# Performance work log

Measured on AMD Instinct MI355X. Metric: run time of the kernel, lower is better.

Reference implementation:

```python
import jax, jax.numpy as jnp
import numpy as np

B, N, D, L = 64, 512, 256, 4


def setup_inputs() -> dict:
    key = jax.random.key(0)
    ks = jax.random.split(key, 10)
    scale = 1.0 / np.sqrt(D)
    x = jax.random.normal(ks[0], (B, N, D), dtype=jnp.float32)
    adj = (jax.random.uniform(ks[1], (B, N, N)) < 0.1).astype(jnp.float32)
    return {
        "x": x,
        "adj": adj,
        "w_attn_w": jax.random.normal(ks[2], (L, D, D), dtype=jnp.float32) * scale,
        "w_attn_b": jnp.zeros((L, D), dtype=jnp.float32),
        "lin0_w": jax.random.normal(ks[3], (L, D, D), dtype=jnp.float32) * scale,
        "lin0_b": jnp.zeros((L, D), dtype=jnp.float32),
        "lin1_w": jax.random.normal(ks[4], (L, D, D), dtype=jnp.float32) * scale,
        "lin1_b": jnp.zeros((L, D), dtype=jnp.float32),
        "final_w": jax.random.normal(ks[5], (D, D), dtype=jnp.float32) * scale,
        "final_b": jnp.zeros((D,), dtype=jnp.float32),
    }


def reference(x, adj, w_attn_w, w_attn_b, lin0_w, lin0_b, lin1_w, lin1_b, final_w, final_b):
    # set self-loops on the adjacency diagonal (in-place in the torch code)
    idx = jnp.arange(N)
    adj = adj.at[:, idx, idx].set(1.0)
    eye = 1e-5 * jnp.eye(N, dtype=x.dtype)
    attls = []
    for l in range(L):
        x0 = x
        # q = w_attn[l](x): torch Linear is x @ W.T + b, W: [out,in]
        q = jnp.einsum('bnd,od->bno', x, w_attn_w[l]) + w_attn_b[l]
        adj_attn = jax.nn.sigmoid(jnp.einsum('bij,bkj->bik', q, x))  # [B,N,N]
        adj_attn = (adj_attn + eye) * adj
        adj_attn = adj_attn / jnp.sum(adj_attn, axis=-1, keepdims=True)
        attls.append(adj_attn)
        x = jnp.einsum('bij,bjd->bid', adj_attn, x)
        x = jax.nn.relu(jnp.einsum('bnd,od->bno', x, lin0_w[l]) + lin0_b[l])
        x = jax.nn.relu(jnp.einsum('bnd,od->bno', x, lin1_w[l]) + lin1_b[l])
        x = x + x0
    x = jnp.einsum('bnd,od->bno', x, final_w) + final_b
    return (x, jnp.stack(attls))
```

## Files before the change

kernel.cpp:

```cpp
#include <hip/hip_runtime.h>
#include <cstdint>

#define B_ 64
#define N_ 512
#define D_ 256
#define L_ 4

typedef __bf16 bf16;
typedef __attribute__((ext_vector_type(8))) __bf16 bf16x8;
typedef __attribute__((ext_vector_type(4))) __bf16 bf16x4;
typedef __attribute__((ext_vector_type(4))) float f32x4;

#define MFMA16(a, b, c) __builtin_amdgcn_mfma_f32_16x16x32_bf16((a), (b), (c), 0, 0, 0)

__device__ __forceinline__ float sigmoidf_(float z) {
  return 1.0f / (1.0f + __expf(-z));
}


#define UIDX(u) (((size_t)(u)) * 64 + lane)

__global__ __launch_bounds__(256) void pack_w(
    const float* __restrict__ src, bf16* __restrict__ dst)
{
  const int tid = threadIdx.x, lane = tid & 63;
  const int U = blockIdx.x * 4 + (tid >> 6);
  const int m = U >> 7, u = U & 127;
  const int r16 = u >> 3, kc = u & 7;
  const int row = r16 * 16 + (lane & 15);
  const int k0 = kc * 32 + (lane >> 4) * 8;
  const float* s = src + (size_t)m * D_ * D_ + (size_t)row * D_ + k0;
  const float4 v0 = *(const float4*)s;
  const float4 v1 = *(const float4*)(s + 4);
  bf16x8 o;
  o[0] = (bf16)v0.x; o[1] = (bf16)v0.y; o[2] = (bf16)v0.z; o[3] = (bf16)v0.w;
  o[4] = (bf16)v1.x; o[5] = (bf16)v1.y; o[6] = (bf16)v1.z; o[7] = (bf16)v1.w;
  ((bf16x8*)dst)[(size_t)U * 64 + lane] = o;
}

__global__ __launch_bounds__(256) void init_pack(
    const float* __restrict__ x, bf16* __restrict__ xbpk, bf16* __restrict__ xTpk)
{
  const int tid = threadIdx.x, lane = tid & 63;
  const int U = blockIdx.x * 4 + (tid >> 6);
  const int b = U >> 9, u = U & 511;
  if (u < 256) {
    const int n = (u >> 3) * 16 + (lane & 15);
    const int d = (u & 7) * 32 + (lane >> 4) * 8;
    const float* s = x + ((size_t)(b * N_ + n)) * D_ + d;
    const float4 v0 = *(const float4*)s;
    const float4 v1 = *(const float4*)(s + 4);
    bf16x8 o;
    o[0] = (bf16)v0.x; o[1] = (bf16)v0.y; o[2] = (bf16)v0.z; o[3] = (bf16)v0.w;
    o[4] = (bf16)v1.x; o[5] = (bf16)v1.y; o[6] = (bf16)v1.z; o[7] = (bf16)v1.w;
    ((bf16x8*)xbpk)[((size_t)b * 256 + u) * 64 + lane] = o;
  } else {
    const int u2 = u - 256;
    const int d = (u2 >> 4) * 16 + (lane & 15);
    const int n = (u2 & 15) * 32 + (lane >> 4) * 8;
    bf16x8 o;
#pragma unroll
    for (int e = 0; e < 8; ++e)
      o[e] = (bf16)x[((size_t)(b * N_ + n + e)) * D_ + d];
    ((bf16x8*)xTpk)[((size_t)b * 256 + u2) * 64 + lane] = o;
  }
}

__global__ __launch_bounds__(512, 1) void gat_layer(
    const bf16* __restrict__ xbpk_in, const bf16* __restrict__ xTpk_in,
    bf16* __restrict__ xbpk_out, bf16* __restrict__ xTpk_out,
    const bf16* __restrict__ Wap, const float* __restrict__ ba,
    const bf16* __restrict__ W0p, const float* __restrict__ b0,
    const bf16* __restrict__ W1p, const float* __restrict__ b1,
    const float* __restrict__ adj, const unsigned short* __restrict__ bits_in,
    unsigned short* __restrict__ bits_out, float* __restrict__ outA)
{
  __shared__ bf16 qs[64 * 264];
  __shared__ bf16 xps[64 * 520];
  __shared__ float psum[8][64];
  __shared__ float rinvs[64];
  __shared__ unsigned int bits_s[1024];

  const int tid = threadIdx.x, w = tid >> 6, lane = tid & 63;
  const int l16 = lane & 15, quad = lane >> 4;
  const int wg = blockIdx.x;
  const int lid = (wg & 7) * 64 + (wg >> 3);
  const int b = lid >> 3;
  const int row0 = (lid & 7) * 64;

  const bf16x8* Xbp = (const bf16x8*)xbpk_in + (size_t)b * 16384;
  const bf16x8* Xtp = (const bf16x8*)xTpk_in + (size_t)b * 16384;
  bf16x8* XbpO = (bf16x8*)xbpk_out + (size_t)b * 16384;
  bf16x8* XtpO = (bf16x8*)xTpk_out + (size_t)b * 16384;
  const bf16x8* Wa8 = (const bf16x8*)Wap;
  const bf16x8* W08 = (const bf16x8*)W0p;
  const bf16x8* W18 = (const bf16x8*)W1p;

  if (bits_in) {
#pragma unroll
    for (int e = 0; e < 2; ++e) {
      const int t = tid + e * 512;
      bits_s[t] = ((const unsigned int*)bits_in)[((size_t)b * N_ + row0) * 16 + t];
    }
  }

  {
    f32x4 acc0[4][2] = {};
#pragma unroll
    for (int ks = 0; ks < 8; ++ks) {
      bf16x8 af[4];
#pragma unroll
      for (int m = 0; m < 4; ++m)
        af[m] = Xbp[UIDX(((row0 >> 4) + m) * 8 + ks)];
      bf16x8 bw[2];
#pragma unroll
      for (int i = 0; i < 2; ++i)
        bw[i] = Wa8[UIDX((2 * w + i) * 8 + ks)];
#pragma unroll
      for (int m = 0; m < 4; ++m)
#pragma unroll
        for (int i = 0; i < 2; ++i) acc0[m][i] = MFMA16(af[m], bw[i], acc0[m][i]);
    }
#pragma unroll
    for (int m = 0; m < 4; ++m)
#pragma unroll
      for (int i = 0; i < 2; ++i) {
        const int col = 32 * w + 16 * i + l16;
        const float bv = ba[col];
#pragma unroll
        for (int r = 0; r < 4; ++r)
          qs[(16 * m + quad * 4 + r) * 264 + col] = (bf16)(acc0[m][i][r] + bv);
      }
  }
  __syncthreads();

  float p[4][4] = {};
  {
    f32x4 acc1[4][4] = {};
#pragma unroll
    for (int ks = 0; ks < 8; ++ks) {
      bf16x8 af[4];
#pragma unroll
      for (int m = 0; m < 4; ++m)
        af[m] = *(const bf16x8*)&qs[(16 * m + l16) * 264 + ks * 32 + quad * 8];
      bf16x8 bx[4];
#pragma unroll
      for (int jt = 0; jt < 4; ++jt)
        bx[jt] = Xbp[UIDX((4 * w + jt) * 8 + ks)];
#pragma unroll
      for (int m = 0; m < 4; ++m)
#pragma unroll
        for (int jt = 0; jt < 4; ++jt)
          acc1[m][jt] = MFMA16(af[m], bx[jt], acc1[m][jt]);
    }
#pragma unroll
    for (int jt = 0; jt < 4; ++jt) {
      const int lcol = 64 * w + jt * 16 + l16;
      const int piece = 4 * w + jt;
#pragma unroll
      for (int m = 0; m < 4; ++m)
#pragma unroll
        for (int r = 0; r < 4; ++r) {
          const int row = 16 * m + quad * 4 + r;
          const int grow = row0 + row;
          float av;
          if (bits_in) {
            const unsigned short m16 = ((const unsigned short*)bits_s)[row * 32 + piece];
            av = (float)((m16 >> l16) & 1);
          } else {
            av = __builtin_nontemporal_load(
                adj + ((size_t)b * N_ + grow) * N_ + lcol);
          }
          const bool diag = (grow == lcol);
          if (bits_out) {
            const unsigned long long bal = __ballot(diag || av != 0.0f);
            if (l16 == 0)
              bits_out[((size_t)b * N_ + row0 + 16 * m + 4 * quad + r) * 32 + piece] =
                  (unsigned short)((bal >> (quad * 16)) & 0xFFFFull);
          }
          const float sg = sigmoidf_(acc1[m][jt][r]);
          const float v = diag ? (sg + 1e-5f) : sg * av;
          const bf16 bv = (bf16)v;
          xps[row * 520 + lcol] = bv;
          p[m][r] += (float)bv;
        }
    }
  }
#pragma unroll
  for (int m = 0; m < 4; ++m)
#pragma unroll
    for (int r = 0; r < 4; ++r) {
#pragma unroll
      for (int msk = 1; msk < 16; msk <<= 1) p[m][r] += __shfl_xor(p[m][r], msk, 64);
    }
  if (l16 == 0) {
#pragma unroll
    for (int m = 0; m < 4; ++m)
#pragma unroll
      for (int r = 0; r < 4; ++r) psum[w][16 * m + quad * 4 + r] = p[m][r];
  }
  __syncthreads();
  if (tid < 64) {
    float s = 0.0f;
#pragma unroll
    for (int ww = 0; ww < 8; ++ww) s += psum[ww][tid];
    rinvs[tid] = 1.0f / s;
  }
  __syncthreads();

  const size_t abase = ((size_t)b * N_ + row0) * N_;
#pragma unroll
  for (int e = 0; e < 16; ++e) {
    const int idx = tid + e * 512;
    const int row = idx >> 7, c4 = (idx & 127) * 4;
    const float ri = rinvs[row];
    bf16x4 pv = *(const bf16x4*)&xps[row * 520 + c4];
    f32x4 nv;
    nv[0] = (float)pv[0] * ri; nv[1] = (float)pv[1] * ri;
    nv[2] = (float)pv[2] * ri; nv[3] = (float)pv[3] * ri;
    __builtin_nontemporal_store(nv, (f32x4*)(outA + abase + (size_t)row * N_ + c4));
    bf16x4 o;
    o[0] = (bf16)nv[0]; o[1] = (bf16)nv[1]; o[2] = (bf16)nv[2]; o[3] = (bf16)nv[3];
    *(bf16x4*)&xps[row * 520 + c4] = o;
  }
  __syncthreads();

  {
    f32x4 acc3[4][2] = {};
#pragma unroll
    for (int ks = 0; ks < 16; ++ks) {
      bf16x8 af[4];
#pragma unroll
      for (int m = 0; m < 4; ++m)
        af[m] = *(const bf16x8*)&xps[(16 * m + l16) * 520 + ks * 32 + quad * 8];
      bf16x8 bt[2];
#pragma unroll
      for (int i = 0; i < 2; ++i)
        bt[i] = Xtp[UIDX((2 * w + i) * 16 + ks)];
#pragma unroll
      for (int m = 0; m < 4; ++m)
#pragma unroll
        for (int i = 0; i < 2; ++i) acc3[m][i] = MFMA16(af[m], bt[i], acc3[m][i]);
    }
#pragma unroll
    for (int m = 0; m < 4; ++m)
#pragma unroll
      for (int i = 0; i < 2; ++i) {
        const int d = 32 * w + 16 * i + l16;
#pragma unroll
        for (int r = 0; r < 4; ++r)
          qs[(16 * m + quad * 4 + r) * 264 + d] = (bf16)acc3[m][i][r];
      }
  }
  __syncthreads();

  {
    f32x4 acc[4][2] = {};
#pragma unroll
    for (int ks = 0; ks < 8; ++ks) {
      bf16x8 af[4];
#pragma unroll
      for (int m = 0; m < 4; ++m)
        af[m] = *(const bf16x8*)&qs[(16 * m + l16) * 264 + ks * 32 + quad * 8];
      bf16x8 bw[2];
#pragma unroll
      for (int i = 0; i < 2; ++i)
        bw[i] = W08[UIDX((2 * w + i) * 8 + ks)];
#pragma unroll
      for (int m = 0; m < 4; ++m)
#pragma unroll
        for (int i = 0; i < 2; ++i) acc[m][i] = MFMA16(af[m], bw[i], acc[m][i]);
    }
#pragma unroll
    for (int m = 0; m < 4; ++m)
#pragma unroll
      for (int i = 0; i < 2; ++i) {
        const int col = 32 * w + 16 * i + l16;
        const float bv = b0[col];
#pragma unroll
        for (int r = 0; r < 4; ++r)
          xps[(16 * m + quad * 4 + r) * 264 + col] = (bf16)fmaxf(acc[m][i][r] + bv, 0.0f);
      }
  }
  __syncthreads();

  {
#pragma unroll
    for (int j = 0; j < 4; ++j) {
      const int uu = w * 4 + j;
      const int rr = uu >> 3, kc = uu & 7;
      const bf16x8 v = Xbp[UIDX(((row0 >> 4) + rr) * 8 + kc)];
      *(bf16x8*)&qs[(rr * 16 + l16) * 264 + kc * 32 + quad * 8] = v;
    }
    f32x4 acc[4][2] = {};
#pragma unroll
    for (int ks = 0; ks < 8; ++ks) {
      bf16x8 af[4];
#pragma unroll
      for (int m = 0; m < 4; ++m)
        af[m] = *(const bf16x8*)&xps[(16 * m + l16) * 264 + ks * 32 + quad * 8];
      bf16x8 bw[2];
#pragma unroll
      for (int i = 0; i < 2; ++i)
        bw[i] = W18[UIDX((2 * w + i) * 8 + ks)];
#pragma unroll
      for (int m = 0; m < 4; ++m)
#pragma unroll
        for (int i = 0; i < 2; ++i) acc[m][i] = MFMA16(af[m], bw[i], acc[m][i]);
    }
    __syncthreads();

#pragma unroll
    for (int m = 0; m < 4; ++m)
#pragma unroll
      for (int i = 0; i < 2; ++i) {
        const int d = 32 * w + 16 * i + l16;
        const float bv = b1[d];
#pragma unroll
        for (int r = 0; r < 4; ++r) {
          const int nl = 16 * m + quad * 4 + r;
          const float x0 = (float)qs[nl * 264 + d];
          const float t2 = fmaxf(acc[m][i][r] + bv, 0.0f) + x0;
          qs[nl * 264 + d] = (bf16)t2;
        }
      }
    __syncthreads();

#pragma unroll
    for (int j = 0; j < 4; ++j) {
      const int uu = w * 4 + j;
      const int rr = uu >> 3, kc = uu & 7;
      const bf16x8 v = *(const bf16x8*)&qs[(rr * 16 + l16) * 264 + kc * 32 + quad * 8];
      XbpO[UIDX(((row0 >> 4) + rr) * 8 + kc)] = v;
    }
#pragma unroll
    for (int j = 0; j < 4; ++j) {
      const int uu = w * 4 + j;
      const int d16 = uu >> 1, nk = uu & 1;
      const int d = d16 * 16 + l16;
      bf16x8 v;
#pragma unroll
      for (int e = 0; e < 8; ++e)
        v[e] = qs[(nk * 32 + quad * 8 + e) * 264 + d];
      XtpO[UIDX(d16 * 16 + (row0 >> 5) + nk)] = v;
    }
  }
}

__global__ __launch_bounds__(256, 4) void final_proj(
    const bf16* __restrict__ xbpk, const bf16* __restrict__ Wfp,
    const float* __restrict__ bfv, float* __restrict__ outX)
{
  const int tid = threadIdx.x, w = tid >> 6, lane = tid & 63;
  const int l16 = lane & 15, quad = lane >> 4;
  const int wg = blockIdx.x;
  const int lid = (wg & 7) * 128 + (wg >> 3);
  const int row0g = lid * 32;
  const int b = row0g >> 9, n0 = row0g & 511;
  const bf16x8* Xbp = (const bf16x8*)xbpk + (size_t)b * 16384;
  const bf16x8* Wf8 = (const bf16x8*)Wfp;
  f32x4 acc[2][4] = {};
#pragma unroll
  for (int ks = 0; ks < 8; ++ks) {
    bf16x8 af[2];
#pragma unroll
    for (int m = 0; m < 2; ++m)
      af[m] = Xbp[UIDX(((n0 >> 4) + m) * 8 + ks)];
    bf16x8 bw[4];
#pragma unroll
    for (int i = 0; i < 4; ++i)
      bw[i] = Wf8[UIDX((4 * w + i) * 8 + ks)];
#pragma unroll
    for (int m = 0; m < 2; ++m)
#pragma unroll
      for (int i = 0; i < 4; ++i) acc[m][i] = MFMA16(af[m], bw[i], acc[m][i]);
  }
#pragma unroll
  for (int m = 0; m < 2; ++m)
#pragma unroll
    for (int i = 0; i < 4; ++i) {
      const int col = 64 * w + 16 * i + l16;
      const float bv = bfv[col];
#pragma unroll
      for (int r = 0; r < 4; ++r) {
        const size_t R = (size_t)row0g + 16 * m + quad * 4 + r;
        __builtin_nontemporal_store(acc[m][i][r] + bv, outX + R * D_ + col);
      }
    }
}

extern "C" void kernel_launch(void* const* d_in, const int* in_sizes, int n_in,
                              void* d_out, int out_size, void* d_ws, size_t ws_size,
                              hipStream_t stream)
{
  const float* x_in  = (const float*)d_in[0];
  const float* adj   = (const float*)d_in[1];
  const float* wattn = (const float*)d_in[2];
  const float* battn = (const float*)d_in[3];
  const float* w0    = (const float*)d_in[4];
  const float* b0    = (const float*)d_in[5];
  const float* w1    = (const float*)d_in[6];
  const float* b1    = (const float*)d_in[7];
  const float* wf    = (const float*)d_in[8];
  const float* bfin  = (const float*)d_in[9];

  float* out_x    = (float*)d_out;
  float* out_attn = out_x + (size_t)B_ * N_ * D_;

  const size_t XBN = (size_t)B_ * N_ * D_;
  const int DD2 = D_ * D_;
  bf16* wb   = (bf16*)d_ws;
  bf16* xbp0 = wb + 13 * DD2;
  bf16* xtp0 = xbp0 + XBN;
  bf16* xbp1 = xtp0 + XBN;
  bf16* xtp1 = xbp1 + XBN;
  unsigned short* bits = (unsigned short*)(xtp1 + XBN);

  pack_w<<<dim3(4 * 32), 256, 0, stream>>>(wattn, wb);
  pack_w<<<dim3(4 * 32), 256, 0, stream>>>(w0, wb + 4 * DD2);
  pack_w<<<dim3(4 * 32), 256, 0, stream>>>(w1, wb + 8 * DD2);
  pack_w<<<dim3(1 * 32), 256, 0, stream>>>(wf, wb + 12 * DD2);

  init_pack<<<dim3(8192), 256, 0, stream>>>(x_in, xbp0, xtp0);

  bf16* xbps[2] = {xbp0, xbp1};
  bf16* xtps[2] = {xtp0, xtp1};
  for (int l = 0; l < L_; ++l) {
    const int pi = l & 1, po = 1 - pi;
    gat_layer<<<dim3((N_ / 64) * B_), 512, 0, stream>>>(
        xbps[pi], xtps[pi], xbps[po], xtps[po],
        wb + l * DD2, battn + l * D_,
        wb + (4 + l) * DD2, b0 + l * D_,
        wb + (8 + l) * DD2, b1 + l * D_,
        adj, (l == 0) ? nullptr : bits, (l == 0) ? bits : nullptr,
        out_attn + (size_t)l * B_ * N_ * N_);
  }
  final_proj<<<dim3((B_ * N_) / 32), 256, 0, stream>>>(
      xbps[0], wb + 12 * DD2, bfin, out_x);
}
```

Before: 725.0 us.

## Double row tile per workgroup to 128 rows with aliased shared buffers

Each gat_layer workgroup now processes 128 rows instead of 64, halving the grid and doubling register accumulators. Per-batch X, Xt and weight fragments are loaded once per 128 rows, which halves the global/L2 reads of the shared operands. Shared memory is reorganized into two 128x264 bf16 buffers that are reused across stages, with the 128x512 attention tile split across them. The trade-off is fewer workgroups (256 instead of 512), more register pressure, and extra barriers, which may reduce latency hiding.

```diff
diff --git a/kernel.cpp b/kernel.cpp
--- a/kernel.cpp
+++ b/kernel.cpp
@@ -75,18 +75,18 @@
     const float* __restrict__ adj, const unsigned short* __restrict__ bits_in,
     unsigned short* __restrict__ bits_out, float* __restrict__ outA)
 {
-  __shared__ bf16 qs[64 * 264];
-  __shared__ bf16 xps[64 * 520];
-  __shared__ float psum[8][64];
-  __shared__ float rinvs[64];
-  __shared__ unsigned int bits_s[1024];
+  __shared__ bf16 bufA[128 * 264];
+  __shared__ bf16 bufB[128 * 264];
+  __shared__ float psum[8][128];
+  __shared__ float rinvs[128];
+  __shared__ unsigned int bits_s[2048];
 
   const int tid = threadIdx.x, w = tid >> 6, lane = tid & 63;
   const int l16 = lane & 15, quad = lane >> 4;
   const int wg = blockIdx.x;
-  const int lid = (wg & 7) * 64 + (wg >> 3);
-  const int b = lid >> 3;
-  const int row0 = (lid & 7) * 64;
+  const int lid = (wg & 7) * 32 + (wg >> 3);
+  const int b = lid >> 2;
+  const int row0 = (lid & 3) * 128;
 
   const bf16x8* Xbp = (const bf16x8*)xbpk_in + (size_t)b * 16384;
   const bf16x8* Xtp = (const bf16x8*)xTpk_in + (size_t)b * 16384;
@@ -98,67 +98,73 @@
 
   if (bits_in) {
 #pragma unroll
-    for (int e = 0; e < 2; ++e) {
+    for (int e = 0; e < 4; ++e) {
       const int t = tid + e * 512;
       bits_s[t] = ((const unsigned int*)bits_in)[((size_t)b * N_ + row0) * 16 + t];
     }
   }
 
   {
-    f32x4 acc0[4][2] = {};
+#pragma unroll
+    for (int j = 0; j < 8; ++j) {
+      const int uu = w * 8 + j;
+      const bf16x8 v = Xbp[UIDX(((row0 >> 4) + (uu >> 3)) * 8 + (uu & 7))];
+      *(bf16x8*)&bufB[uu * 512 + lane * 8] = v;
+    }
+    __syncthreads();
+    f32x4 acc0[8][2] = {};
 #pragma unroll
     for (int ks = 0; ks < 8; ++ks) {
-      bf16x8 af[4];
-#pragma unroll
-      for (int m = 0; m < 4; ++m)
-        af[m] = Xbp[UIDX(((row0 >> 4) + m) * 8 + ks)];
       bf16x8 bw[2];
 #pragma unroll
       for (int i = 0; i < 2; ++i)
         bw[i] = Wa8[UIDX((2 * w + i) * 8 + ks)];
 #pragma unroll
-      for (int m = 0; m < 4; ++m)
-#pragma unroll
-        for (int i = 0; i < 2; ++i) acc0[m][i] = MFMA16(af[m], bw[i], acc0[m][i]);
-    }
-#pragma unroll
-    for (int m = 0; m < 4; ++m)
+      for (int m = 0; m < 8; ++m) {
+        const bf16x8 af = *(const bf16x8*)&bufB[(m * 8 + ks) * 512 + lane * 8];
+#pragma unroll
+        for (int i = 0; i < 2; ++i) acc0[m][i] = MFMA16(af, bw[i], acc0[m][i]);
+      }
+    }
+    __syncthreads();
+#pragma unroll
+    for (int m = 0; m < 8; ++m)
 #pragma unroll
       for (int i = 0; i < 2; ++i) {
         const int col = 32 * w + 16 * i + l16;
         const float bv = ba[col];
 #pragma unroll
         for (int r = 0; r < 4; ++r)
-          qs[(16 * m + quad * 4 + r) * 264 + col] = (bf16)(acc0[m][i][r] + bv);
-      }
-  }
-  __syncthreads();
-
-  float p[4][4] = {};
+          bufA[(16 * m + quad * 4 + r) * 264 + col] = (bf16)(acc0[m][i][r] + bv);
+      }
+  }
+  __syncthreads();
+
+  float p[8][4] = {};
   {
-    f32x4 acc1[4][4] = {};
+    f32x4 acc1[8][4] = {};
 #pragma unroll
     for (int ks = 0; ks < 8; ++ks) {
-      bf16x8 af[4];
-#pragma unroll
-      for (int m = 0; m < 4; ++m)
-        af[m] = *(const bf16x8*)&qs[(16 * m + l16) * 264 + ks * 32 + quad * 8];
       bf16x8 bx[4];
 #pragma unroll
       for (int jt = 0; jt < 4; ++jt)
         bx[jt] = Xbp[UIDX((4 * w + jt) * 8 + ks)];
 #pragma unroll
-      for (int m = 0; m < 4; ++m)
+      for (int m = 0; m < 8; ++m) {
+        const bf16x8 af = *(const bf16x8*)&bufA[(16 * m + l16) * 264 + ks * 32 + quad * 8];
 #pragma unroll
         for (int jt = 0; jt < 4; ++jt)
-          acc1[m][jt] = MFMA16(af[m], bx[jt], acc1[m][jt]);
-    }
+          acc1[m][jt] = MFMA16(af, bx[jt], acc1[m][jt]);
+      }
+    }
+    __syncthreads();
+
 #pragma unroll
     for (int jt = 0; jt < 4; ++jt) {
       const int lcol = 64 * w + jt * 16 + l16;
       const int piece = 4 * w + jt;
 #pragma unroll
-      for (int m = 0; m < 4; ++m)
+      for (int m = 0; m < 8; ++m)
 #pragma unroll
         for (int r = 0; r < 4; ++r) {
           const int row = 16 * m + quad * 4 + r;
@@ -175,19 +181,20 @@
           if (bits_out) {
             const unsigned long long bal = __ballot(diag || av != 0.0f);
             if (l16 == 0)
-              bits_out[((size_t)b * N_ + row0 + 16 * m + 4 * quad + r) * 32 + piece] =
+              bits_out[((size_t)b * N_ + grow) * 32 + piece] =
                   (unsigned short)((bal >> (quad * 16)) & 0xFFFFull);
           }
           const float sg = sigmoidf_(acc1[m][jt][r]);
           const float v = diag ? (sg + 1e-5f) : sg * av;
           const bf16 bv = (bf16)v;
-          xps[row * 520 + lcol] = bv;
-          p[m][r] += (float)bv;
+          if (row < 64) bufB[row * 520 + lcol] = bv;
+          else          bufA[(row - 64) * 520 + lcol] = bv;
+          p[m][r] += (float)v;
         }
     }
   }
 #pragma unroll
-  for (int m = 0; m < 4; ++m)
+  for (int m = 0; m < 8; ++m)
 #pragma unroll
     for (int r = 0; r < 4; ++r) {
 #pragma unroll
@@ -195,12 +202,12 @@
     }
   if (l16 == 0) {
 #pragma unroll
-    for (int m = 0; m < 4; ++m)
+    for (int m = 0; m < 8; ++m)
 #pragma unroll
       for (int r = 0; r < 4; ++r) psum[w][16 * m + quad * 4 + r] = p[m][r];
   }
   __syncthreads();
-  if (tid < 64) {
+  if (tid < 128) {
     float s = 0.0f;
 #pragma unroll
     for (int ww = 0; ww < 8; ++ww) s += psum[ww][tid];
@@ -210,108 +217,106 @@
 
   const size_t abase = ((size_t)b * N_ + row0) * N_;
 #pragma unroll
-  for (int e = 0; e < 16; ++e) {
+  for (int e = 0; e < 32; ++e) {
     const int idx = tid + e * 512;
     const int row = idx >> 7, c4 = (idx & 127) * 4;
     const float ri = rinvs[row];
-    bf16x4 pv = *(const bf16x4*)&xps[row * 520 + c4];
+    bf16* cell = (row < 64) ? &bufB[row * 520 + c4] : &bufA[(row - 64) * 520 + c4];
+    bf16x4 pv = *(const bf16x4*)cell;
     f32x4 nv;
     nv[0] = (float)pv[0] * ri; nv[1] = (float)pv[1] * ri;
     nv[2] = (float)pv[2] * ri; nv[3] = (float)pv[3] * ri;
     __builtin_nontemporal_store(nv, (f32x4*)(outA + abase + (size_t)row * N_ + c4));
     bf16x4 o;
     o[0] = (bf16)nv[0]; o[1] = (bf16)nv[1]; o[2] = (bf16)nv[2]; o[3] = (bf16)nv[3];
-    *(bf16x4*)&xps[row * 520 + c4] = o;
+    *(bf16x4*)cell = o;
   }
   __syncthreads();
 
   {
-    f32x4 acc3[4][2] = {};
+    f32x4 acc3[8][2] = {};
 #pragma unroll
     for (int ks = 0; ks < 16; ++ks) {
-      bf16x8 af[4];
-#pragma unroll
-      for (int m = 0; m < 4; ++m)
-        af[m] = *(const bf16x8*)&xps[(16 * m + l16) * 520 + ks * 32 + quad * 8];
       bf16x8 bt[2];
 #pragma unroll
       for (int i = 0; i < 2; ++i)
         bt[i] = Xtp[UIDX((2 * w + i) * 16 + ks)];
 #pragma unroll
-      for (int m = 0; m < 4; ++m)
-#pragma unroll
-        for (int i = 0; i < 2; ++i) acc3[m][i] = MFMA16(af[m], bt[i], acc3[m][i]);
-    }
-#pragma unroll
-    for (int m = 0; m < 4; ++m)
+      for (int m = 0; m < 8; ++m) {
+        const bf16x8 af = (m < 4)
+            ? *(const bf16x8*)&bufB[(16 * m + l16) * 520 + ks * 32 + quad * 8]
+            : *(const bf16x8*)&bufA[(16 * (m - 4) + l16) * 520 + ks * 32 + quad * 8];
+#pragma unroll
+        for (int i = 0; i < 2; ++i) acc3[m][i] = MFMA16(af, bt[i], acc3[m][i]);
+      }
+    }
+    __syncthreads();
+#pragma unroll
+    for (int m = 0; m < 8; ++m)
 #pragma unroll
       for (int i = 0; i < 2; ++i) {
         const int d = 32 * w + 16 * i + l16;
 #pragma unroll
         for (int r = 0; r < 4; ++r)
-          qs[(16 * m + quad * 4 + r) * 264 + d] = (bf16)acc3[m][i][r];
+          bufA[(16 * m + quad * 4 + r) * 264 + d] = (bf16)acc3[m][i][r];
       }
   }
   __syncthreads();
 
   {
-    f32x4 acc[4][2] = {};
+    f32x4 acc[8][2] = {};
 #pragma unroll
     for (int ks = 0; ks < 8; ++ks) {
-      bf16x8 af[4];
-#pragma unroll
-      for (int m = 0; m < 4; ++m)
-        af[m] = *(const bf16x8*)&qs[(16 * m + l16) * 264 + ks * 32 + quad * 8];
       bf16x8 bw[2];
 #pragma unroll
       for (int i = 0; i < 2; ++i)
         bw[i] = W08[UIDX((2 * w + i) * 8 + ks)];
 #pragma unroll
-      for (int m = 0; m < 4; ++m)
-#pragma unroll
-        for (int i = 0; i < 2; ++i) acc[m][i] = MFMA16(af[m], bw[i], acc[m][i]);
-    }
-#pragma unroll
-    for (int m = 0; m < 4; ++m)
+      for (int m = 0; m < 8; ++m) {
+        const bf16x8 af = *(const bf16x8*)&bufA[(16 * m + l16) * 264 + ks * 32 + quad * 8];
+#pragma unroll
+        for (int i = 0; i < 2; ++i) acc[m][i] = MFMA16(af, bw[i], acc[m][i]);
+      }
+    }
+#pragma unroll
+    for (int m = 0; m < 8; ++m)
 #pragma unroll
       for (int i = 0; i < 2; ++i) {
         const int col = 32 * w + 16 * i + l16;
         const float bv = b0[col];
 #pragma unroll
         for (int r = 0; r < 4; ++r)
-          xps[(16 * m + quad * 4 + r) * 264 + col] = (bf16)fmaxf(acc[m][i][r] + bv, 0.0f);
+          bufB[(16 * m + quad * 4 + r) * 264 + col] = (bf16)fmaxf(acc[m][i][r] + bv, 0.0f);
       }
   }
   __syncthreads();
 
   {
 #pragma unroll
-    for (int j = 0; j < 4; ++j) {
-      const int uu = w * 4 + j;
+    for (int j = 0; j < 8; ++j) {
+      const int uu = w * 8 + j;
       const int rr = uu >> 3, kc = uu & 7;
       const bf16x8 v = Xbp[UIDX(((row0 >> 4) + rr) * 8 + kc)];
-      *(bf16x8*)&qs[(rr * 16 + l16) * 264 + kc * 32 + quad * 8] = v;
-    }
-    f32x4 acc[4][2] = {};
+      *(bf16x8*)&bufA[(rr * 16 + l16) * 264 + kc * 32 + quad * 8] = v;
+    }
+    f32x4 acc[8][2] = {};
 #pragma unroll
     for (int ks = 0; ks < 8; ++ks) {
-      bf16x8 af[4];
-#pragma unroll
-      for (int m = 0; m < 4; ++m)
-        af[m] = *(const bf16x8*)&xps[(16 * m + l16) * 264 + ks * 32 + quad * 8];
       bf16x8 bw[2];
 #pragma unroll
       for (int i = 0; i < 2; ++i)
         bw[i] = W18[UIDX((2 * w + i) * 8 + ks)];
 #pragma unroll
-      for (int m = 0; m < 4; ++m)
-#pragma unroll
-        for (int i = 0; i < 2; ++i) acc[m][i] = MFMA16(af[m], bw[i], acc[m][i]);
-    }
-    __syncthreads();
-
-#pragma unroll
-    for (int m = 0; m < 4; ++m)
+      for (int m = 0; m < 8; ++m) {
+        const bf16x8 af = *(const bf16x8*)&bufB[(16 * m + l16) * 264 + ks * 32 + quad * 8];
+#pragma unroll
+        for (int i = 0; i < 2; ++i) acc[m][i] = MFMA16(af, bw[i], acc[m][i]);
+      }
+    }
+    __syncthreads();
+
+#pragma unroll
+    for (int m = 0; m < 8; ++m)
 #pragma unroll
       for (int i = 0; i < 2; ++i) {
         const int d = 32 * w + 16 * i + l16;
@@ -319,29 +324,29 @@
 #pragma unroll
         for (int r = 0; r < 4; ++r) {
           const int nl = 16 * m + quad * 4 + r;
-          const float x0 = (float)qs[nl * 264 + d];
+          const float x0 = (float)bufA[nl * 264 + d];
           const float t2 = fmaxf(acc[m][i][r] + bv, 0.0f) + x0;
-          qs[nl * 264 + d] = (bf16)t2;
+          bufA[nl * 264 + d] = (bf16)t2;
         }
       }
     __syncthreads();
 
 #pragma unroll
-    for (int j = 0; j < 4; ++j) {
-      const int uu = w * 4 + j;
+    for (int j = 0; j < 8; ++j) {
+      const int uu = w * 8 + j;
       const int rr = uu >> 3, kc = uu & 7;
-      const bf16x8 v = *(const bf16x8*)&qs[(rr * 16 + l16) * 264 + kc * 32 + quad * 8];
+      const bf16x8 v = *(const bf16x8*)&bufA[(rr * 16 + l16) * 264 + kc * 32 + quad * 8];
       XbpO[UIDX(((row0 >> 4) + rr) * 8 + kc)] = v;
     }
 #pragma unroll
-    for (int j = 0; j < 4; ++j) {
-      const int uu = w * 4 + j;
-      const int d16 = uu >> 1, nk = uu & 1;
+    for (int j = 0; j < 8; ++j) {
+      const int uu = w * 8 + j;
+      const int d16 = uu >> 2, nk = uu & 3;
       const int d = d16 * 16 + l16;
       bf16x8 v;
 #pragma unroll
       for (int e = 0; e < 8; ++e)
-        v[e] = qs[(nk * 32 + quad * 8 + e) * 264 + d];
+        v[e] = bufA[(nk * 32 + quad * 8 + e) * 264 + d];
       XtpO[UIDX(d16 * 16 + (row0 >> 5) + nk)] = v;
     }
   }
@@ -427,7 +432,7 @@
   bf16* xtps[2] = {xtp0, xtp1};
   for (int l = 0; l < L_; ++l) {
     const int pi = l & 1, po = 1 - pi;
-    gat_layer<<<dim3((N_ / 64) * B_), 512, 0, stream>>>(
+    gat_layer<<<dim3((N_ / 128) * B_), 512, 0, stream>>>(
         xbps[pi], xtps[pi], xbps[po], xtps[po],
         wb + l * DD2, battn + l * D_,
         wb + (4 + l) * DD2, b0 + l * D_,
```

Measured after the change: 733.5 us. No clear change (+1.2%).
